# Performance work log

Hardware: AMD Instinct MI355X
Metric: run time of the kernel (lower is better)

The kernel has to match this reference:

```python
import jax, jax.numpy as jnp
import numpy as np

B, S, SE, H, NH = 1, 2048, 2048, 1024, 16
HD = H // NH
INNER = 4 * H
EPS = 1e-5


def layer_norm(x, g, b):
    mu = jnp.mean(x, axis=-1, keepdims=True)
    var = jnp.mean(jnp.square(x - mu), axis=-1, keepdims=True)
    return (x - mu) * jax.lax.rsqrt(var + EPS) * g + b


def split_heads(x):  # [B,T,H] -> [B,NH,T,HD]
    b, t, _ = x.shape
    return x.reshape(b, t, NH, HD).transpose(0, 2, 1, 3)


def merge_heads(x):  # [B,NH,T,HD] -> [B,T,H]
    b, nh, t, hd = x.shape
    return x.transpose(0, 2, 1, 3).reshape(b, t, nh * hd)


def setup_inputs() -> dict:
    key = jax.random.key(0)
    ks = jax.random.split(key, 16)
    n = lambda k, shp: (jax.random.normal(k, shp, jnp.float32) * 0.02)
    return {
        "hidden_states": jax.random.normal(ks[0], (B, S, H), jnp.float32),
        "encoder_hidden_states": jax.random.normal(ks[1], (B, SE, H), jnp.float32),
        "scorer_logits": jax.random.normal(ks[2], (B, SE), jnp.float32),
        "ln1_g": jnp.ones((H,), jnp.float32), "ln1_b": jnp.zeros((H,), jnp.float32),
        "c_attn_w": n(ks[3], (H, 3 * H)), "c_attn_b": jnp.zeros((3 * H,), jnp.float32),
        "attn_proj_w": n(ks[4], (H, H)), "attn_proj_b": jnp.zeros((H,), jnp.float32),
        "lnx_g": jnp.ones((H,), jnp.float32), "lnx_b": jnp.zeros((H,), jnp.float32),
        "q_attn_w": n(ks[5], (H, H)), "q_attn_b": jnp.zeros((H,), jnp.float32),
        "x_kv_w": n(ks[6], (H, 2 * H)), "x_kv_b": jnp.zeros((2 * H,), jnp.float32),
        "x_proj_w": n(ks[7], (H, H)), "x_proj_b": jnp.zeros((H,), jnp.float32),
        "ln2_g": jnp.ones((H,), jnp.float32), "ln2_b": jnp.zeros((H,), jnp.float32),
        "fc_w": n(ks[8], (H, INNER)), "fc_b": jnp.zeros((INNER,), jnp.float32),
        "mlp_proj_w": n(ks[9], (INNER, H)), "mlp_proj_b": jnp.zeros((H,), jnp.float32),
    }


def _attn_core(q, k, v, extra_bias=None, causal_bool=False, tril_diag2_additive=False):
    # q,k,v: [B,NH,T,HD]; eager attention, materializes full score matrix (faithful to source)
    w = jnp.einsum("bhqd,bhkd->bhqk", q, k) / jnp.sqrt(jnp.asarray(HD, q.dtype))
    ql, kl = q.shape[-2], k.shape[-2]
    neg = jnp.finfo(w.dtype).min
    if causal_bool:
        mask = jnp.tril(jnp.ones((ql, kl), bool))  # self-attn boolean causal mask
        w = jnp.where(mask[None, None], w, neg)
    if tril_diag2_additive:
        cm = jnp.tril(jnp.ones((ql, kl), w.dtype), k=2)  # limit_cross_attn: tril diagonal=2
        w = w + jnp.where(cm == 0, neg, jnp.zeros((), w.dtype))[None, None]
    if extra_bias is not None:
        w = w + extra_bias[:, None, None, :]  # scorer_logits additive per-key bias
    w = jax.nn.softmax(w, axis=-1)
    return jnp.einsum("bhqk,bhkd->bhqd", w, v)


def reference(hidden_states, encoder_hidden_states, scorer_logits,
              ln1_g, ln1_b, c_attn_w, c_attn_b, attn_proj_w, attn_proj_b,
              lnx_g, lnx_b, q_attn_w, q_attn_b, x_kv_w, x_kv_b, x_proj_w, x_proj_b,
              ln2_g, ln2_b, fc_w, fc_b, mlp_proj_w, mlp_proj_b):
    # --- self attention ---
    residual = hidden_states
    x = layer_norm(hidden_states, ln1_g, ln1_b)
    qkv = x @ c_attn_w + c_attn_b
    q, k, v = jnp.split(qkv, 3, axis=-1)
    a = _attn_core(split_heads(q), split_heads(k), split_heads(v), causal_bool=True)
    a = merge_heads(a) @ attn_proj_w + attn_proj_b
    hidden_states = a + residual
    # --- cross attention (limit_cross_attn=True, scorer_logits bias) ---
    residual = hidden_states
    x = layer_norm(hidden_states, lnx_g, lnx_b)
    q = x @ q_attn_w + q_attn_b
    kv = encoder_hidden_states @ x_kv_w + x_kv_b
    k, v = jnp.split(kv, 2, axis=-1)
    a = _attn_core(split_heads(q), split_heads(k), split_heads(v),
                   extra_bias=scorer_logits, tril_diag2_additive=True)
    a = merge_heads(a) @ x_proj_w + x_proj_b
    hidden_states = residual + a
    # --- MLP (gelu_new = tanh approx) ---
    residual = hidden_states
    x = layer_norm(hidden_states, ln2_g, ln2_b)
    h = jax.nn.gelu(x @ fc_w + fc_b, approximate=True)
    hidden_states = residual + (h @ mlp_proj_w + mlp_proj_b)
    return hidden_states
```

## Files before the change

### kernel.cpp

```cpp
#include <hip/hip_runtime.h>
#include <stdint.h>

#define H     1024
#define S     2048
#define SEQE  2048
#define NHEAD 16
#define HD    64
#define INNER 4096
#define EPSLN 1e-5f
#define LOG2E 1.44269504089f
#define SCALE2 (0.125f * LOG2E)

typedef __attribute__((ext_vector_type(8))) short short8;
typedef __attribute__((ext_vector_type(4))) float floatx4;

__device__ __forceinline__ float b2f(unsigned short u){
  union { unsigned int i; float f; } v; v.i = ((unsigned int)u) << 16; return v.f;
}
__device__ __forceinline__ unsigned short f2b(float f){
  union { float f; unsigned int i; } v; v.f = f;
  unsigned int x = v.i;
  unsigned int r = (x + 0x7FFFu + ((x >> 16) & 1u)) >> 16;
  return (unsigned short)r;
}
__device__ __forceinline__ float gelu_tanh(float x){
  float x3 = x*x*x;
  float t = tanhf(0.7978845608028654f*(x + 0.044715f*x3));
  return 0.5f*x*(1.0f+t);
}

__device__ __forceinline__ void gld16(const unsigned short* g, unsigned short* l){
  __builtin_amdgcn_global_load_lds(
      (const __attribute__((address_space(1))) unsigned int*)g,
      (__attribute__((address_space(3))) unsigned int*)l,
      16, 0, 0);
}

__global__ __launch_bounds__(256) void k_sniff(
    const unsigned short* __restrict__ p, int* __restrict__ flag){
  __shared__ int any;
  if (threadIdx.x == 0) any = 0;
  __syncthreads();
  int bad = 0;
  for (int i = threadIdx.x; i < 8192; i += 256){
    float v = b2f(p[i]);
    if (!(fabsf(v) < 1e6f)) bad = 1;
  }
  if (bad) any = 1;
  __syncthreads();
  if (threadIdx.x == 0) flag[0] = any;
}

__global__ __launch_bounds__(256) void k_cvt(
    const void* __restrict__ src, unsigned short* __restrict__ dst, int n,
    const int* __restrict__ flag){
  int i = blockIdx.x * 256 + threadIdx.x;
  if (i < n)
    dst[i] = flag[0] ? f2b(((const float*)src)[i]) : ((const unsigned short*)src)[i];
}

struct SmallCvt {
  const void* src[16];
  unsigned short* dst[16];
  int n[16];
};
__global__ __launch_bounds__(256) void k_cvt_small(SmallCvt sc, const int* __restrict__ flag){
  int t = blockIdx.x;
  int fl = flag[0];
  const float* sf = (const float*)sc.src[t];
  const unsigned short* sb = (const unsigned short*)sc.src[t];
  unsigned short* d = sc.dst[t];
  for (int i = threadIdx.x; i < sc.n[t]; i += 256)
    d[i] = fl ? f2b(sf[i]) : sb[i];
}

__global__ __launch_bounds__(256) void k_transpose(
    const void* __restrict__ srcv, unsigned short* __restrict__ dst,
    int R, int C, const int* __restrict__ flag){
  __shared__ unsigned short t[32][33];
  const float* sf = (const float*)srcv;
  const unsigned short* sb = (const unsigned short*)srcv;
  int fl = flag[0];
  int bc = blockIdx.x * 32, br = blockIdx.y * 32;
  int tx = threadIdx.x, ty = threadIdx.y;
  #pragma unroll
  for (int i = 0; i < 4; i++){
    size_t idx = (size_t)(br + ty + i*8) * C + bc + tx;
    t[ty + i*8][tx] = fl ? f2b(sf[idx]) : sb[idx];
  }
  __syncthreads();
  #pragma unroll
  for (int i = 0; i < 4; i++)
    dst[(size_t)(bc + ty + i*8) * R + br + tx] = t[tx][ty + i*8];
}

__global__ __launch_bounds__(256) void k_resid_init(
    const void* __restrict__ in, float* __restrict__ out, int n,
    const int* __restrict__ flag){
  int i = blockIdx.x * 256 + threadIdx.x;
  if (i < n)
    out[i] = flag[0] ? ((const float*)in)[i] : b2f(((const unsigned short*)in)[i]);
}

__global__ __launch_bounds__(256) void k_layernorm(
    const float* __restrict__ x,
    const unsigned short* __restrict__ g, const unsigned short* __restrict__ bb,
    unsigned short* __restrict__ y){
  __shared__ float scratch[4];
  int row = blockIdx.x, tid = threadIdx.x;
  float v[4];
  #pragma unroll
  for (int i=0;i<4;i++) v[i] = x[(size_t)row*H + tid + i*256];
  float s = v[0]+v[1]+v[2]+v[3];
  for (int o=32;o;o>>=1) s += __shfl_xor(s,o,64);
  int wid = tid>>6, lane = tid&63;
  if (lane==0) scratch[wid]=s;
  __syncthreads();
  float mu = (scratch[0]+scratch[1]+scratch[2]+scratch[3]) * (1.0f/H);
  __syncthreads();
  float q = 0.f;
  #pragma unroll
  for (int i=0;i<4;i++){ float d=v[i]-mu; q += d*d; }
  for (int o=32;o;o>>=1) q += __shfl_xor(q,o,64);
  if (lane==0) scratch[wid]=q;
  __syncthreads();
  float var = (scratch[0]+scratch[1]+scratch[2]+scratch[3]) * (1.0f/H);
  float rstd = rsqrtf(var + EPSLN);
  #pragma unroll
  for (int i=0;i<4;i++){
    int idx = tid + i*256;
    float o = (v[i]-mu)*rstd*b2f(g[idx]) + b2f(bb[idx]);
    y[(size_t)row*H + idx] = f2b(o);
  }
}

__global__ __launch_bounds__(256) void k_gemm64(
    const unsigned short* __restrict__ A, const unsigned short* __restrict__ BT,
    const unsigned short* __restrict__ bias,
    unsigned short* __restrict__ outb, float* __restrict__ resid,
    int M, int N, int K, int mode, const int* __restrict__ flag,
    int vcol0, unsigned short* __restrict__ vtout)
{
  __shared__ __align__(16) unsigned short As[64*64];
  __shared__ __align__(16) unsigned short Bs[128*64];
  int tid = threadIdx.x;
  int bm0 = blockIdx.y * 64, bn0 = blockIdx.x * 128;
  int wid = tid >> 6, lane = tid & 63;
  int wm = (wid & 1) * 32, wn = (wid >> 1) * 64;
  int fl = (mode == 3) ? flag[0] : 0;
  floatx4 acc[2][4] = {};

  const unsigned short* gp[6];
  unsigned short* lp[6];
  int lrow = lane >> 3, lchunk = (lane & 7) ^ lrow;
  #pragma unroll
  for (int t = 0; t < 6; t++){
    int seg = wid * 6 + t;
    if (seg < 8){
      gp[t] = A + (size_t)(bm0 + seg*8 + lrow) * K + lchunk*8;
      lp[t] = &As[seg * 512];
    } else {
      int s = seg - 8;
      gp[t] = BT + (size_t)(bn0 + s*8 + lrow) * K + lchunk*8;
      lp[t] = &Bs[s * 512];
    }
  }

  int mrow = lane & 15, quad = lane >> 4;
  for (int kt = 0; kt < K; kt += 64){
    #pragma unroll
    for (int t = 0; t < 6; t++) gld16(gp[t] + kt, lp[t]);
    __syncthreads();
    #pragma unroll
    for (int k2 = 0; k2 < 2; k2++){
      short8 af[2], bf[4];
      #pragma unroll
      for (int i = 0; i < 2; i++){
        int r = wm + i*16 + mrow;
        int slot = (k2*4 + quad) ^ (r & 7);
        af[i] = *(const short8*)&As[r*64 + slot*8];
      }
      #pragma unroll
      for (int j = 0; j < 4; j++){
        int r = wn + j*16 + mrow;
        int slot = (k2*4 + quad) ^ (r & 7);
        bf[j] = *(const short8*)&Bs[r*64 + slot*8];
      }
      #pragma unroll
      for (int i = 0; i < 2; i++){
        #pragma unroll
        for (int j = 0; j < 4; j++){
          acc[i][j] = __builtin_amdgcn_mfma_f32_16x16x32_bf16(af[i], bf[j], acc[i][j], 0,0,0);
        }
      }
    }
    __syncthreads();
  }

  int colb = mrow, rowb = quad * 4;
  #pragma unroll
  for (int i=0;i<2;i++){
    #pragma unroll
    for (int j=0;j<4;j++){
      int col = bn0 + wn + j*16 + colb;
      float bv = b2f(bias[col]);
      int row0 = bm0 + wm + i*16 + rowb;
      if (mode == 4 && col >= vcol0){
        ushort4 uv;
        uv.x = f2b(acc[i][j][0] + bv);
        uv.y = f2b(acc[i][j][1] + bv);
        uv.z = f2b(acc[i][j][2] + bv);
        uv.w = f2b(acc[i][j][3] + bv);
        *(ushort4*)(vtout + (size_t)(col - vcol0)*M + row0) = uv;
      } else {
        #pragma unroll
        for (int rr=0;rr<4;rr++){
          int row = row0 + rr;
          float v = acc[i][j][rr] + bv;
          size_t off = (size_t)row*N + col;
          if      (mode == 0 || mode == 4){ outb[off] = f2b(v); }
          else if (mode == 1){ outb[off] = f2b(gelu_tanh(v)); }
          else if (mode == 2){ resid[off] += v; }
          else {
            float o = v + resid[off];
            if (fl) ((float*)outb)[off] = o;
            else    outb[off] = f2b(o);
          }
        }
      }
    }
  }
}

template<int CA, int SCOR>
__global__ __launch_bounds__(256) void k_flash2(
    const unsigned short* __restrict__ qb, int qstride,
    const unsigned short* __restrict__ kb, int kstride,
    const unsigned short* __restrict__ vt,
    const unsigned short* __restrict__ scorer,
    unsigned short* __restrict__ obuf, float* __restrict__ mlbuf, int TOTS)
{
  int t = blockIdx.x, h = blockIdx.y, sp = blockIdx.z;
  int klmax0 = 64*t + 64 + CA; if (klmax0 > S) klmax0 = S;
  int nch = (klmax0 + 63) >> 6;
  int nsp = (nch + 7) >> 3;
  if (sp >= nsp) return;
  int base = 0;
  for (int i = 0; i < t; i++){
    int km = 64*i + 64 + CA; if (km > S) km = S;
    base += (((km + 63) >> 6) + 7) >> 3;
  }
  int pidx = h*TOTS + base + sp;
  int c0 = sp*8, c1 = c0 + 8; if (c1 > nch) c1 = nch;

  __shared__ __align__(16) unsigned short Ks[64*64];
  __shared__ __align__(16) unsigned short VTs[64*64];
  __shared__ __align__(16) unsigned short Ps[4][16*72];
  __shared__ float scs[64];
  int tid = threadIdx.x;
  int q0 = t*64;
  int w = tid >> 6, lane = tid & 63;
  int cn = lane & 15, quad = lane >> 4, kq = quad * 8;
  unsigned short* Pw = Ps[w];
  int srow0 = w*16;
  int lr = lane >> 3;
  int lc = ((lane & 7) ^ lr) * 8;
  const unsigned short* kg0 = kb + (size_t)(srow0 + lr) * kstride + h*HD + lc;
  const unsigned short* kg1 = kb + (size_t)(srow0 + 8 + lr) * kstride + h*HD + lc;
  const unsigned short* vg0 = vt + (size_t)(h*HD + srow0 + lr) * S + lc;
  const unsigned short* vg1 = vt + (size_t)(h*HD + srow0 + 8 + lr) * S + lc;
  unsigned short* kl0 = &Ks[srow0 * 64];
  unsigned short* kl1 = &Ks[(srow0 + 8) * 64];
  unsigned short* vl0 = &VTs[srow0 * 64];
  unsigned short* vl1 = &VTs[(srow0 + 8) * 64];

  const unsigned short* qrow = qb + (size_t)(q0 + w*16 + cn) * qstride + h*HD;
  short8 qf0 = *(const short8*)(qrow + kq);
  short8 qf1 = *(const short8*)(qrow + kq + 32);
  floatx4 oacc[4] = {};
  float l_lane[4] = {0,0,0,0};
  float m_w = -1.0e38f;
  int qmr = q0 + w*16 + quad*4;

  for (int ci = c0; ci < c1; ci++){
    int kc = ci * 64;
    __syncthreads();
    gld16(kg0 + (size_t)kc * kstride, kl0);
    gld16(kg1 + (size_t)kc * kstride, kl1);
    gld16(vg0 + kc, vl0);
    gld16(vg1 + kc, vl1);
    if (SCOR && tid < 64) scs[tid] = b2f(scorer[kc + tid]) * LOG2E;
    __syncthreads();

    floatx4 sv[4] = {};
    #pragma unroll
    for (int t4=0;t4<4;t4++){
      int rr = t4*16 + cn;
      int s0 = ((quad    ) ^ (rr & 7)) * 8;
      int s1 = ((quad + 4) ^ (rr & 7)) * 8;
      short8 b0 = *(const short8*)&Ks[rr*64 + s0];
      short8 b1 = *(const short8*)&Ks[rr*64 + s1];
      sv[t4] = __builtin_amdgcn_mfma_f32_16x16x32_bf16(qf0, b0, sv[t4], 0,0,0);
      sv[t4] = __builtin_amdgcn_mfma_f32_16x16x32_bf16(qf1, b1, sv[t4], 0,0,0);
    }

    float vals[16];
    float lmax = -1.0e38f;
    bool needmask = (kc + 63 > q0 + w*16 + CA);
    #pragma unroll
    for (int t4=0;t4<4;t4++){
      #pragma unroll
      for (int r=0;r<4;r++){
        float s = sv[t4][r] * SCALE2;
        if (SCOR) s += scs[t4*16 + cn];
        if (needmask){
          int kn = kc + t4*16 + cn;
          s = (kn <= qmr + r + CA) ? s : -1.0e38f;
        }
        vals[t4*4+r] = s;
        lmax = fmaxf(lmax, s);
      }
    }
    #pragma unroll
    for (int o=1;o<64;o<<=1) lmax = fmaxf(lmax, __shfl_xor(lmax, o, 64));
    if (lmax > m_w){
      float al = exp2f(m_w - lmax);
      m_w = lmax;
      #pragma unroll
      for (int r=0;r<4;r++) l_lane[r] *= al;
      #pragma unroll
      for (int t2=0;t2<4;t2++){
        #pragma unroll
        for (int r=0;r<4;r++) oacc[t2][r] *= al;
      }
    }
    #pragma unroll
    for (int t4=0;t4<4;t4++){
      #pragma unroll
      for (int r=0;r<4;r++){
        float e = exp2f(vals[t4*4+r] - m_w);
        l_lane[r] += e;
        Pw[(quad*4+r)*72 + t4*16 + cn] = f2b(e);
      }
    }
    short8 pf0 = *(const short8*)&Pw[cn*72 + kq];
    short8 pf1 = *(const short8*)&Pw[cn*72 + kq + 32];
    #pragma unroll
    for (int t2=0;t2<4;t2++){
      int rr = t2*16 + cn;
      int s0 = ((quad    ) ^ (rr & 7)) * 8;
      int s1 = ((quad + 4) ^ (rr & 7)) * 8;
      short8 v0 = *(const short8*)&VTs[rr*64 + s0];
      short8 v1 = *(const short8*)&VTs[rr*64 + s1];
      oacc[t2] = __builtin_amdgcn_mfma_f32_16x16x32_bf16(pf0, v0, oacc[t2], 0,0,0);
      oacc[t2] = __builtin_amdgcn_mfma_f32_16x16x32_bf16(pf1, v1, oacc[t2], 0,0,0);
    }
  }

  float lrow[4];
  #pragma unroll
  for (int r=0;r<4;r++){
    float l = l_lane[r];
    l += __shfl_xor(l,1,64); l += __shfl_xor(l,2,64);
    l += __shfl_xor(l,4,64); l += __shfl_xor(l,8,64);
    lrow[r] = l;
  }
  size_t ob = (size_t)pidx*4096 + (size_t)(w*16 + quad*4)*64;
  #pragma unroll
  for (int t2=0;t2<4;t2++){
    #pragma unroll
    for (int r=0;r<4;r++)
      obuf[ob + r*64 + t2*16 + cn] = f2b(oacc[t2][r]);
  }
  if (cn == 0){
    #pragma unroll
    for (int r=0;r<4;r++){
      int row64 = w*16 + quad*4 + r;
      mlbuf[((size_t)pidx*64 + row64)*2]   = m_w;
      mlbuf[((size_t)pidx*64 + row64)*2+1] = lrow[r];
    }
  }
}

template<int CA>
__global__ __launch_bounds__(256) void k_comb(
    const unsigned short* __restrict__ obuf, const float* __restrict__ mlbuf,
    unsigned short* __restrict__ out, int TOTS)
{
  int h = blockIdx.y;
  int row = blockIdx.x*16 + (threadIdx.x >> 4);
  int d0 = (threadIdx.x & 15) * 4;
  int t = row >> 6;
  int klmax0 = 64*t + 64 + CA; if (klmax0 > S) klmax0 = S;
  int nch = (klmax0 + 63) >> 6;
  int nsp = (nch + 7) >> 3;
  int base = 0;
  for (int i = 0; i < t; i++){
    int km = 64*i + 64 + CA; if (km > S) km = S;
    base += (((km + 63) >> 6) + 7) >> 3;
  }
  int row64 = row & 63;
  float mp[4], lp[4];
  float M = -1.0e38f;
  for (int p = 0; p < nsp; p++){
    int pi = h*TOTS + base + p;
    mp[p] = mlbuf[((size_t)pi*64 + row64)*2];
    lp[p] = mlbuf[((size_t)pi*64 + row64)*2+1];
    M = fmaxf(M, mp[p]);
  }
  float L = 0.f;
  float o0=0.f,o1=0.f,o2=0.f,o3=0.f;
  for (int p = 0; p < nsp; p++){
    int pi = h*TOTS + base + p;
    float wgt = exp2f(mp[p] - M);
    L += lp[p]*wgt;
    const unsigned short* op = obuf + (size_t)pi*4096 + row64*64 + d0;
    o0 += b2f(op[0])*wgt; o1 += b2f(op[1])*wgt;
    o2 += b2f(op[2])*wgt; o3 += b2f(op[3])*wgt;
  }
  float inv = 1.0f / L;
  size_t oo = (size_t)row*H + h*HD + d0;
  out[oo]   = f2b(o0*inv); out[oo+1] = f2b(o1*inv);
  out[oo+2] = f2b(o2*inv); out[oo+3] = f2b(o3*inv);
}

extern "C" void kernel_launch(void* const* d_in, const int* in_sizes, int n_in,
                              void* d_out, int out_size, void* d_ws, size_t ws_size,
                              hipStream_t stream)
{
  const void* hs          = d_in[0];
  const void* enc         = d_in[1];
  const void* scorer      = d_in[2];
  const void* ln1_g       = d_in[3];
  const void* ln1_b       = d_in[4];
  const void* c_attn_w    = d_in[5];
  const void* c_attn_b    = d_in[6];
  const void* attn_proj_w = d_in[7];
  const void* attn_proj_b = d_in[8];
  const void* lnx_g       = d_in[9];
  const void* lnx_b       = d_in[10];
  const void* q_attn_w    = d_in[11];
  const void* q_attn_b    = d_in[12];
  const void* x_kv_w      = d_in[13];
  const void* x_kv_b      = d_in[14];
  const void* x_proj_w    = d_in[15];
  const void* x_proj_b    = d_in[16];
  const void* ln2_g       = d_in[17];
  const void* ln2_b       = d_in[18];
  const void* fc_w        = d_in[19];
  const void* fc_b        = d_in[20];
  const void* mlp_proj_w  = d_in[21];
  const void* mlp_proj_b  = d_in[22];
  unsigned short* out = (unsigned short*)d_out;

  char* ws = (char*)d_ws; size_t off = 0;
  auto alloc = [&](size_t bytes)->void*{
    void* p = ws + off; off += (bytes + 255) & ~(size_t)255; return p;
  };
  unsigned short* wT_cattn = (unsigned short*)alloc((size_t)3072*1024*2);
  unsigned short* wT_aproj = (unsigned short*)alloc((size_t)1024*1024*2);
  unsigned short* wT_qattn = (unsigned short*)alloc((size_t)1024*1024*2);
  unsigned short* wT_xkv   = (unsigned short*)alloc((size_t)2048*1024*2);
  unsigned short* wT_xproj = (unsigned short*)alloc((size_t)1024*1024*2);
  unsigned short* wT_fc    = (unsigned short*)alloc((size_t)4096*1024*2);
  unsigned short* wT_mlp   = (unsigned short*)alloc((size_t)1024*4096*2);
  unsigned short* enc_c    = (unsigned short*)alloc((size_t)SEQE*H*2);
  unsigned short* canon    = (unsigned short*)alloc((size_t)32768*2);
  unsigned short* xln      = (unsigned short*)alloc((size_t)S*H*2);
  unsigned short* qkv      = (unsigned short*)alloc((size_t)S*3*H*2);
  unsigned short* attnout  = (unsigned short*)alloc((size_t)S*H*2);
  unsigned short* q2       = (unsigned short*)alloc((size_t)S*H*2);
  unsigned short* kvbuf    = (unsigned short*)alloc((size_t)SEQE*2*H*2);
  unsigned short* vt_self  = (unsigned short*)alloc((size_t)H*S*2);
  unsigned short* vt_cross = (unsigned short*)alloc((size_t)H*SEQE*2);
  unsigned short* fcbuf    = (unsigned short*)alloc((size_t)S*INNER*2);
  float*          hidden   = (float*)alloc((size_t)S*H*4);
  int*            flag     = (int*)alloc(256);

  unsigned short* obuf  = fcbuf;
  float*          mlbuf = (float*)(fcbuf + (size_t)16*83*4096);

  unsigned short* p = canon;
  auto carve = [&](int n)->unsigned short*{ unsigned short* q = p; p += n; return q; };
  unsigned short* c_ln1g = carve(1024); unsigned short* c_ln1b = carve(1024);
  unsigned short* c_catb = carve(3072); unsigned short* c_aprb = carve(1024);
  unsigned short* c_lnxg = carve(1024); unsigned short* c_lnxb = carve(1024);
  unsigned short* c_qatb = carve(1024); unsigned short* c_xkvb = carve(2048);
  unsigned short* c_xprb = carve(1024); unsigned short* c_ln2g = carve(1024);
  unsigned short* c_ln2b = carve(1024); unsigned short* c_fcb  = carve(4096);
  unsigned short* c_mlpb = carve(1024); unsigned short* c_scor = carve(2048);

  k_sniff<<<1, 256, 0, stream>>>((const unsigned short*)hs, flag);
  k_resid_init<<<(S*H)/256, 256, 0, stream>>>(hs, hidden, S*H, flag);

  dim3 tb(32,8);
  k_transpose<<<dim3(3072/32,1024/32), tb, 0, stream>>>(c_attn_w,    wT_cattn, 1024, 3072, flag);
  k_transpose<<<dim3(1024/32,1024/32), tb, 0, stream>>>(attn_proj_w, wT_aproj, 1024, 1024, flag);
  k_transpose<<<dim3(1024/32,1024/32), tb, 0, stream>>>(q_attn_w,    wT_qattn, 1024, 1024, flag);
  k_transpose<<<dim3(2048/32,1024/32), tb, 0, stream>>>(x_kv_w,      wT_xkv,   1024, 2048, flag);
  k_transpose<<<dim3(1024/32,1024/32), tb, 0, stream>>>(x_proj_w,    wT_xproj, 1024, 1024, flag);
  k_transpose<<<dim3(4096/32,1024/32), tb, 0, stream>>>(fc_w,        wT_fc,    1024, 4096, flag);
  k_transpose<<<dim3(1024/32,4096/32), tb, 0, stream>>>(mlp_proj_w,  wT_mlp,   4096, 1024, flag);

  k_cvt<<<(SEQE*H)/256, 256, 0, stream>>>(enc, enc_c, SEQE*H, flag);
  SmallCvt sc{};
  const void* ssrc[14] = {ln1_g, ln1_b, c_attn_b, attn_proj_b, lnx_g, lnx_b,
                          q_attn_b, x_kv_b, x_proj_b, ln2_g, ln2_b, fc_b,
                          mlp_proj_b, scorer};
  unsigned short* sdst[14] = {c_ln1g, c_ln1b, c_catb, c_aprb, c_lnxg, c_lnxb,
                              c_qatb, c_xkvb, c_xprb, c_ln2g, c_ln2b, c_fcb,
                              c_mlpb, c_scor};
  int sn[14] = {1024,1024,3072,1024,1024,1024,1024,2048,1024,1024,1024,4096,1024,2048};
  for (int i=0;i<14;i++){ sc.src[i]=ssrc[i]; sc.dst[i]=sdst[i]; sc.n[i]=sn[i]; }
  k_cvt_small<<<14, 256, 0, stream>>>(sc, flag);

  k_layernorm<<<S, 256, 0, stream>>>(hidden, c_ln1g, c_ln1b, xln);
  k_gemm64<<<dim3(3072/128, S/64), 256, 0, stream>>>(xln, wT_cattn, c_catb,
      qkv, nullptr, S, 3072, 1024, 4, flag, 2048, vt_self);
  k_flash2<0,0><<<dim3(32, NHEAD, 4), 256, 0, stream>>>(
      qkv, 3*H, qkv + 1024, 3*H, vt_self, nullptr, obuf, mlbuf, 80);
  k_comb<0><<<dim3(S/16, NHEAD), 256, 0, stream>>>(obuf, mlbuf, attnout, 80);
  k_gemm64<<<dim3(1024/128, S/64), 256, 0, stream>>>(attnout, wT_aproj, c_aprb,
      nullptr, hidden, S, 1024, 1024, 2, flag, 0, nullptr);

  k_layernorm<<<S, 256, 0, stream>>>(hidden, c_lnxg, c_lnxb, xln);
  k_gemm64<<<dim3(1024/128, S/64), 256, 0, stream>>>(xln, wT_qattn, c_qatb,
      q2, nullptr, S, 1024, 1024, 0, flag, 0, nullptr);
  k_gemm64<<<dim3(2048/128, SEQE/64), 256, 0, stream>>>(enc_c, wT_xkv, c_xkvb,
      kvbuf, nullptr, SEQE, 2048, 1024, 4, flag, 1024, vt_cross);
  k_flash2<2,1><<<dim3(32, NHEAD, 4), 256, 0, stream>>>(
      q2, H, kvbuf, 2*H, vt_cross, c_scor, obuf, mlbuf, 83);
  k_comb<2><<<dim3(S/16, NHEAD), 256, 0, stream>>>(obuf, mlbuf, attnout, 83);
  k_gemm64<<<dim3(1024/128, S/64), 256, 0, stream>>>(attnout, wT_xproj, c_xprb,
      nullptr, hidden, S, 1024, 1024, 2, flag, 0, nullptr);

  k_layernorm<<<S, 256, 0, stream>>>(hidden, c_ln2g, c_ln2b, xln);
  k_gemm64<<<dim3(INNER/128, S/64), 256, 0, stream>>>(xln, wT_fc, c_fcb,
      fcbuf, nullptr, S, INNER, 1024, 1, flag, 0, nullptr);
  k_gemm64<<<dim3(1024/128, S/64), 256, 0, stream>>>(fcbuf, wT_mlp, c_mlpb,
      out, hidden, S, 1024, INNER, 3, flag, 0, nullptr);
}
```

Baseline: 546.8 us.

## Double-buffer LDS tiles in GEMM to overlap global loads with MFMA

The 64x128 bf16 GEMM kernel now keeps two LDS buffers for the A and B tiles. The first tile is loaded before the loop. Each iteration issues the next tile's global-to-LDS loads right after the barrier and then runs MFMAs on the current buffer, so the trailing barrier is dropped. The goal is to hide global memory latency behind compute and cut one barrier per K-step. The cost is twice the LDS per block (about 48KB), which can lower occupancy.

```diff
diff --git a/kernel.cpp b/kernel.cpp
--- a/kernel.cpp
+++ b/kernel.cpp
@@ -141,8 +141,8 @@
     int M, int N, int K, int mode, const int* __restrict__ flag,
     int vcol0, unsigned short* __restrict__ vtout)
 {
-  __shared__ __align__(16) unsigned short As[64*64];
-  __shared__ __align__(16) unsigned short Bs[128*64];
+  __shared__ __align__(16) unsigned short As[2][64*64];
+  __shared__ __align__(16) unsigned short Bs[2][128*64];
   int tid = threadIdx.x;
   int bm0 = blockIdx.y * 64, bn0 = blockIdx.x * 128;
   int wid = tid >> 6, lane = tid & 63;
@@ -151,26 +151,39 @@
   floatx4 acc[2][4] = {};
 
   const unsigned short* gp[6];
-  unsigned short* lp[6];
+  int lofs[6];
+  int aseg[6];
   int lrow = lane >> 3, lchunk = (lane & 7) ^ lrow;
   #pragma unroll
   for (int t = 0; t < 6; t++){
     int seg = wid * 6 + t;
     if (seg < 8){
       gp[t] = A + (size_t)(bm0 + seg*8 + lrow) * K + lchunk*8;
-      lp[t] = &As[seg * 512];
+      lofs[t] = seg * 512;
+      aseg[t] = 1;
     } else {
       int s = seg - 8;
       gp[t] = BT + (size_t)(bn0 + s*8 + lrow) * K + lchunk*8;
-      lp[t] = &Bs[s * 512];
-    }
-  }
+      lofs[t] = s * 512;
+      aseg[t] = 0;
+    }
+  }
+
+  #pragma unroll
+  for (int t = 0; t < 6; t++)
+    gld16(gp[t], (aseg[t] ? As[0] : Bs[0]) + lofs[t]);
 
   int mrow = lane & 15, quad = lane >> 4;
-  for (int kt = 0; kt < K; kt += 64){
-    #pragma unroll
-    for (int t = 0; t < 6; t++) gld16(gp[t] + kt, lp[t]);
+  int ib = 0;
+  for (int kt = 0; kt < K; kt += 64, ib ^= 1){
     __syncthreads();
+    if (kt + 64 < K){
+      #pragma unroll
+      for (int t = 0; t < 6; t++)
+        gld16(gp[t] + kt + 64, (aseg[t] ? As[ib^1] : Bs[ib^1]) + lofs[t]);
+    }
+    const unsigned short* Ac = As[ib];
+    const unsigned short* Bc = Bs[ib];
     #pragma unroll
     for (int k2 = 0; k2 < 2; k2++){
       short8 af[2], bf[4];
@@ -178,13 +191,13 @@
       for (int i = 0; i < 2; i++){
         int r = wm + i*16 + mrow;
         int slot = (k2*4 + quad) ^ (r & 7);
-        af[i] = *(const short8*)&As[r*64 + slot*8];
+        af[i] = *(const short8*)&Ac[r*64 + slot*8];
       }
       #pragma unroll
       for (int j = 0; j < 4; j++){
         int r = wn + j*16 + mrow;
         int slot = (k2*4 + quad) ^ (r & 7);
-        bf[j] = *(const short8*)&Bs[r*64 + slot*8];
+        bf[j] = *(const short8*)&Bc[r*64 + slot*8];
       }
       #pragma unroll
       for (int i = 0; i < 2; i++){
@@ -194,7 +207,6 @@
         }
       }
     }
-    __syncthreads();
   }
 
   int colb = mrow, rowb = quad * 4;
```

Result: faster. 517.5 us (-5.4%).
